# Kernel optimization log

Hardware: AMD Instinct MI355X
Metric: run time of the kernel (lower is better)

The kernel has to match this reference:

```python
import jax, jax.numpy as jnp
import numpy as np

N, D, E = 100000, 128, 800000

def setup_inputs() -> dict:
    key = jax.random.key(0)
    k1, k2, k3, k4 = jax.random.split(key, 4)
    z = jax.random.normal(k1, (N, D), dtype=jnp.float32)
    edge_index = jax.random.randint(k2, (2, E), 0, N, dtype=jnp.int64)
    # PyTorch-style init scale for Linear layers (kaiming-uniform-ish via normal is fine for a numeric reference)
    W1 = jax.random.normal(k3, (2 * D, D), dtype=jnp.float32) * (1.0 / np.sqrt(2 * D))
    b1 = jnp.zeros((D,), dtype=jnp.float32)
    W2 = jax.random.normal(k4, (D, 1), dtype=jnp.float32) * (1.0 / np.sqrt(D))
    b2 = jnp.zeros((1,), dtype=jnp.float32)
    return {"z": z, "edge_index": edge_index, "W1": W1, "b1": b1, "W2": W2, "b2": b2}

def reference(z, edge_index, W1, b1, W2, b2):
    # row/col gather of node embeddings
    row, col = edge_index[0], edge_index[1]
    # cat([z[row], z[col]]) @ W1 == z[row] @ W1[:D] + z[col] @ W1[D:]
    # -> avoids materializing the [E, 2D] concatenated tensor
    d = z.shape[1]
    h = z[row] @ W1[:d] + z[col] @ W1[d:] + b1          # [E, D]
    h = jax.nn.relu(h)                                   # Dropout(0.1) is identity in eval mode
    out = h @ W2 + b2                                    # [E, 1]
    return out.squeeze(-1)                               # [E]
```

## Files before the change

kernel.cpp:

```cpp
#include <hip/hip_runtime.h>

#define DDIM 128

typedef __bf16 bf16x8 __attribute__((ext_vector_type(8)));
typedef float  floatx4 __attribute__((ext_vector_type(4)));

__global__ __launch_bounds__(256, 4) void precompute_uv_mfma_q8(
    const float* __restrict__ z, const float* __restrict__ W1,
    const float* __restrict__ b1,
    unsigned char* __restrict__ U8, unsigned char* __restrict__ V8,
    float* __restrict__ u_scale, float* __restrict__ v_scale,
    int N, int nchunks)
{
    __shared__ unsigned short WsF[32 * 64 * 8];

    const int t    = threadIdx.x;
    const int lane = t & 63;
    const int w    = t >> 6;
    const int half = blockIdx.x;
    unsigned char* __restrict__ dst8 = half ? V8 : U8;
    float*         __restrict__ dscl = half ? v_scale : u_scale;
    const float*   __restrict__ Wh   = W1 + (size_t)half * DDIM * DDIM;

    const int mrow = lane & 15;
    const int quad = lane >> 4;
    const int gy   = gridDim.y;

    float4 rx[8];
    auto issue_loads = [&](int ch) {
        int grow = ch * 64 + w * 16 + mrow;
        if (grow > N - 1) grow = N - 1;
        const float* zrow = z + (size_t)grow * DDIM;
        #pragma unroll
        for (int ks = 0; ks < 4; ++ks) {
            const int k0 = ks * 32 + quad * 8;
            rx[2 * ks]     = *(const float4*)(zrow + k0);
            rx[2 * ks + 1] = *(const float4*)(zrow + k0 + 4);
        }
    };

    if (blockIdx.y < nchunks) issue_loads(blockIdx.y);

    {
        const int nlow = lane & 15;
        const int kq   = (lane >> 4) & 3;
        #pragma unroll
        for (int i = 0; i < 8; ++i) {
            const int ntks = w + i * 4;
            const int nt = ntks >> 2, ks = ntks & 3;
            const int n  = nt * 16 + nlow;
            const int kb = ks * 32 + kq * 8;
            float f[8];
            #pragma unroll
            for (int j = 0; j < 8; ++j)
                f[j] = Wh[(kb + j) * DDIM + n];
            unsigned pk[4];
            #pragma unroll
            for (int j = 0; j < 4; ++j)
                asm("v_cvt_pk_bf16_f32 %0, %1, %2"
                    : "=v"(pk[j]) : "v"(f[2 * j]), "v"(f[2 * j + 1]));
            *(uint4*)&WsF[(ntks * 64 + lane) * 8] = *(const uint4*)pk;
        }
    }

    float bval[8];
    #pragma unroll
    for (int nt = 0; nt < 8; ++nt)
        bval[nt] = (half == 0) ? b1[nt * 16 + mrow] : 0.f;

    __syncthreads();

    for (int chunk = blockIdx.y; chunk < nchunks; chunk += gy) {
        bf16x8 afrag[4];
        #pragma unroll
        for (int ks = 0; ks < 4; ++ks) {
            const float4 x0 = rx[2 * ks];
            const float4 x1 = rx[2 * ks + 1];
            unsigned pk[4];
            asm("v_cvt_pk_bf16_f32 %0, %1, %2" : "=v"(pk[0]) : "v"(x0.x), "v"(x0.y));
            asm("v_cvt_pk_bf16_f32 %0, %1, %2" : "=v"(pk[1]) : "v"(x0.z), "v"(x0.w));
            asm("v_cvt_pk_bf16_f32 %0, %1, %2" : "=v"(pk[2]) : "v"(x1.x), "v"(x1.y));
            asm("v_cvt_pk_bf16_f32 %0, %1, %2" : "=v"(pk[3]) : "v"(x1.z), "v"(x1.w));
            afrag[ks] = __builtin_bit_cast(bf16x8, *(const uint4*)pk);
        }

        const int nxt = chunk + gy;
        if (nxt < nchunks) issue_loads(nxt);

        floatx4 acc[8];
        #pragma unroll
        for (int nt = 0; nt < 8; ++nt)
            acc[nt] = (floatx4){bval[nt], bval[nt], bval[nt], bval[nt]};

        #pragma unroll
        for (int ks = 0; ks < 4; ++ks) {
            #pragma unroll
            for (int nt = 0; nt < 8; ++nt) {
                const bf16x8 b = __builtin_bit_cast(bf16x8,
                    *(const uint4*)&WsF[((nt * 4 + ks) * 64 + lane) * 8]);
                acc[nt] = __builtin_amdgcn_mfma_f32_16x16x32_bf16(afrag[ks], b, acc[nt], 0, 0, 0);
            }
        }

        #pragma unroll
        for (int r = 0; r < 4; ++r) {
            float mx = fmaxf(fmaxf(fabsf(acc[0][r]), fabsf(acc[1][r])),
                             fabsf(acc[2][r]));
            mx = fmaxf(fmaxf(mx, fabsf(acc[3][r])), fabsf(acc[4][r]));
            mx = fmaxf(fmaxf(mx, fabsf(acc[5][r])), fabsf(acc[6][r]));
            mx = fmaxf(mx, fabsf(acc[7][r]));
            #pragma unroll
            for (int m = 1; m < 16; m <<= 1)
                mx = fmaxf(mx, __shfl_xor(mx, m, 16));
            mx = fmaxf(mx, 1e-20f);
            const float inv = 127.f * __builtin_amdgcn_rcpf(mx);

            unsigned char bytes[8];
            #pragma unroll
            for (int nt = 0; nt < 8; ++nt) {
                const float fq = fmaf(acc[nt][r], inv, 12583040.0f);
                bytes[nt] = (unsigned char)(__builtin_bit_cast(unsigned, fq) & 0xffu);
            }
            const int grow = chunk * 64 + w * 16 + quad * 4 + r;
            if (grow < N) {
                *(uint2*)&dst8[(size_t)grow * DDIM + mrow * 8] =
                    *(const uint2*)bytes;
                if (mrow == 0) dscl[grow] = mx * (1.f / 127.f);
            }
        }
    }
}

__global__ __launch_bounds__(256) void edge_kernel_i8(
    const int* __restrict__ ei,
    const unsigned char* __restrict__ U8, const unsigned char* __restrict__ V8,
    const float* __restrict__ u_scale, const float* __restrict__ v_scale,
    const float* __restrict__ W2, const float* __restrict__ b2,
    float* __restrict__ out, int E)
{
    const int t  = threadIdx.x;
    const int q  = t & 7;
    const int g0 = (blockIdx.x * 32 + (t >> 3)) * 4;
    if (g0 >= E) return;

    float ww[16];
    #pragma unroll
    for (int k = 0; k < 16; ++k)
        ww[k] = W2[(k & 7) * 16 + 2 * q + (k >> 3)];

    int rows[4], cols[4];
    if (g0 + 3 < E) {
        const int4 r4 = *(const int4*)(ei + g0);
        const int4 c4 = *(const int4*)(ei + (size_t)E + g0);
        rows[0]=r4.x; rows[1]=r4.y; rows[2]=r4.z; rows[3]=r4.w;
        cols[0]=c4.x; cols[1]=c4.y; cols[2]=c4.z; cols[3]=c4.w;
    } else {
        #pragma unroll
        for (int i = 0; i < 4; ++i) {
            const int gi = (g0 + i < E) ? (g0 + i) : (E - 1);
            rows[i] = ei[gi];
            cols[i] = ei[(size_t)E + gi];
        }
    }

    uint4 uu[4], vv[4];
    #pragma unroll
    for (int i = 0; i < 4; ++i)
        uu[i] = *(const uint4*)(U8 + (size_t)rows[i] * DDIM + q * 16);
    #pragma unroll
    for (int i = 0; i < 4; ++i)
        vv[i] = *(const uint4*)(V8 + (size_t)cols[i] * DDIM + q * 16);

    float su[4], sv[4];
    #pragma unroll
    for (int i = 0; i < 4; ++i) { su[i] = u_scale[rows[i]]; sv[i] = v_scale[cols[i]]; }

    const float bias = b2[0];

    float sres[4];
    #pragma unroll
    for (int i = 0; i < 4; ++i) {
        const unsigned uw0 = uu[i].x, uw1 = uu[i].y, uw2 = uu[i].z, uw3 = uu[i].w;
        const unsigned vw0 = vv[i].x, vw1 = vv[i].y, vw2 = vv[i].z, vw3 = vv[i].w;
        const float c = -128.f * (su[i] + sv[i]);
        float s = 0.f;
        #pragma unroll
        for (int k = 0; k < 16; ++k) {
            const unsigned uwk = (k < 4) ? uw0 : (k < 8) ? uw1 : (k < 12) ? uw2 : uw3;
            const unsigned vwk = (k < 4) ? vw0 : (k < 8) ? vw1 : (k < 12) ? vw2 : vw3;
            const float uf = (float)((uwk >> (8 * (k & 3))) & 0xffu);
            const float vf = (float)((vwk >> (8 * (k & 3))) & 0xffu);
            const float h  = fmaf(su[i], uf, fmaf(sv[i], vf, c));
            s = fmaf(fmaxf(h, 0.f), ww[k], s);
        }
        s += __shfl_down(s, 4, 8);
        s += __shfl_down(s, 2, 8);
        s += __shfl_down(s, 1, 8);
        sres[i] = s + bias;
    }

    if (q == 0) {
        if (g0 + 3 < E) {
            float4 o; o.x = sres[0]; o.y = sres[1]; o.z = sres[2]; o.w = sres[3];
            *(float4*)&out[g0] = o;
        } else {
            #pragma unroll
            for (int i = 0; i < 4; ++i)
                if (g0 + i < E) out[g0 + i] = sres[i];
        }
    }
}

__global__ __launch_bounds__(256) void edge_fused_fallback(
    const float* __restrict__ z, const int* __restrict__ ei,
    const float* __restrict__ W1, const float* __restrict__ b1,
    const float* __restrict__ W2, const float* __restrict__ b2,
    float* __restrict__ out, int N, int E)
{
    const int tid  = blockIdx.x * 256 + threadIdx.x;
    const int e    = tid >> 6;
    const int lane = tid & 63;
    if (e >= E) return;

    const int row = ei[e];
    const int col = ei[(size_t)E + e];
    const float* zr = z + (size_t)row * DDIM;
    const float* zc = z + (size_t)col * DDIM;

    float h0 = b1[lane];
    float h1 = b1[lane + 64];
    for (int k = 0; k < DDIM; ++k) {
        const float a = zr[k];
        const float b = zc[k];
        h0 = fmaf(a, W1[k * DDIM + lane],               h0);
        h0 = fmaf(b, W1[(DDIM + k) * DDIM + lane],      h0);
        h1 = fmaf(a, W1[k * DDIM + lane + 64],          h1);
        h1 = fmaf(b, W1[(DDIM + k) * DDIM + lane + 64], h1);
    }
    float s = fmaxf(h0, 0.f) * W2[lane] + fmaxf(h1, 0.f) * W2[lane + 64];
    #pragma unroll
    for (int off = 32; off > 0; off >>= 1)
        s += __shfl_down(s, off, 64);
    if (lane == 0) out[e] = s + b2[0];
}

extern "C" void kernel_launch(void* const* d_in, const int* in_sizes, int n_in,
                              void* d_out, int out_size, void* d_ws, size_t ws_size,
                              hipStream_t stream)
{
    const float* z  = (const float*)d_in[0];
    const int*   ei = (const int*)d_in[1];
    const float* W1 = (const float*)d_in[2];
    const float* b1 = (const float*)d_in[3];
    const float* W2 = (const float*)d_in[4];
    const float* b2 = (const float*)d_in[5];
    float*       out = (float*)d_out;

    const int N = in_sizes[0] / DDIM;
    const int E = in_sizes[1] / 2;

    const size_t n128 = (size_t)N * DDIM;
    const size_t need = 2 * n128 + 2 * (size_t)N * sizeof(float) + 256;
    if (ws_size >= need) {
        unsigned char* U8 = (unsigned char*)d_ws;
        unsigned char* V8 = U8 + n128;
        float* usc = (float*)(((size_t)(V8 + n128) + 255) & ~(size_t)255);
        float* vsc = usc + N;
        const int nchunks = (N + 63) / 64;
        const int gy = nchunks < 640 ? nchunks : 640;
        hipLaunchKernelGGL(precompute_uv_mfma_q8, dim3(2, gy), dim3(256), 0, stream,
                           z, W1, b1, U8, V8, usc, vsc, N, nchunks);
        hipLaunchKernelGGL(edge_kernel_i8, dim3((E + 127) / 128), dim3(256), 0, stream,
                           ei, U8, V8, usc, vsc, W2, b2, out, E);
    } else {
        hipLaunchKernelGGL(edge_fused_fallback, dim3((E + 3) / 4), dim3(256), 0, stream,
                           z, ei, W1, b1, W2, b2, out, N, E);
    }
}
```

Baseline: 139.7 us.

## Stage z tiles through swizzled LDS for coalesced loads in precompute kernel

```diff
diff --git a/kernel.cpp b/kernel.cpp
--- a/kernel.cpp
+++ b/kernel.cpp
@@ -5,7 +5,7 @@
 typedef __bf16 bf16x8 __attribute__((ext_vector_type(8)));
 typedef float  floatx4 __attribute__((ext_vector_type(4)));
 
-__global__ __launch_bounds__(256, 4) void precompute_uv_mfma_q8(
+__global__ __launch_bounds__(256, 2) void precompute_uv_mfma_q8(
     const float* __restrict__ z, const float* __restrict__ W1,
     const float* __restrict__ b1,
     unsigned char* __restrict__ U8, unsigned char* __restrict__ V8,
@@ -13,6 +13,7 @@
     int N, int nchunks)
 {
     __shared__ unsigned short WsF[32 * 64 * 8];
+    __shared__ float As[4][16][128];
 
     const int t    = threadIdx.x;
     const int lane = t & 63;
@@ -25,17 +26,32 @@
     const int mrow = lane & 15;
     const int quad = lane >> 4;
     const int gy   = gridDim.y;
+    const int rsub = lane >> 3;
+    const int usub = lane & 7;
 
     float4 rx[8];
     auto issue_loads = [&](int ch) {
-        int grow = ch * 64 + w * 16 + mrow;
-        if (grow > N - 1) grow = N - 1;
-        const float* zrow = z + (size_t)grow * DDIM;
-        #pragma unroll
-        for (int ks = 0; ks < 4; ++ks) {
-            const int k0 = ks * 32 + quad * 8;
-            rx[2 * ks]     = *(const float4*)(zrow + k0);
-            rx[2 * ks + 1] = *(const float4*)(zrow + k0 + 4);
+        const int base = ch * 64 + w * 16;
+        #pragma unroll
+        for (int rg = 0; rg < 2; ++rg) {
+            int grow = base + 8 * rg + rsub;
+            if (grow > N - 1) grow = N - 1;
+            const float* zrow = z + (size_t)grow * DDIM;
+            #pragma unroll
+            for (int cq = 0; cq < 4; ++cq)
+                rx[rg * 4 + cq] = *(const float4*)(zrow + cq * 32 + usub * 4);
+        }
+    };
+
+    auto write_tile = [&]() {
+        #pragma unroll
+        for (int rg = 0; rg < 2; ++rg) {
+            const int rl = 8 * rg + rsub;
+            #pragma unroll
+            for (int cq = 0; cq < 4; ++cq) {
+                const int pos = cq * 8 + (usub ^ rsub);
+                *(float4*)&As[w][rl][pos * 4] = rx[rg * 4 + cq];
+            }
         }
     };
 
@@ -71,11 +87,17 @@
     __syncthreads();
 
     for (int chunk = blockIdx.y; chunk < nchunks; chunk += gy) {
+        write_tile();
+        const int nxt = chunk + gy;
+        if (nxt < nchunks) issue_loads(nxt);
+
         bf16x8 afrag[4];
         #pragma unroll
         for (int ks = 0; ks < 4; ++ks) {
-            const float4 x0 = rx[2 * ks];
-            const float4 x1 = rx[2 * ks + 1];
+            const int u0 = ks * 8 + ((quad * 2)     ^ (mrow & 7));
+            const int u1 = ks * 8 + ((quad * 2 + 1) ^ (mrow & 7));
+            const float4 x0 = *(const float4*)&As[w][mrow][u0 * 4];
+            const float4 x1 = *(const float4*)&As[w][mrow][u1 * 4];
             unsigned pk[4];
             asm("v_cvt_pk_bf16_f32 %0, %1, %2" : "=v"(pk[0]) : "v"(x0.x), "v"(x0.y));
             asm("v_cvt_pk_bf16_f32 %0, %1, %2" : "=v"(pk[1]) : "v"(x0.z), "v"(x0.w));
@@ -83,9 +105,6 @@
             asm("v_cvt_pk_bf16_f32 %0, %1, %2" : "=v"(pk[3]) : "v"(x1.z), "v"(x1.w));
             afrag[ks] = __builtin_bit_cast(bf16x8, *(const uint4*)pk);
         }
-
-        const int nxt = chunk + gy;
-        if (nxt < nchunks) issue_loads(nxt);
 
         floatx4 acc[8];
         #pragma unroll
@@ -267,7 +286,7 @@
         float* usc = (float*)(((size_t)(V8 + n128) + 255) & ~(size_t)255);
         float* vsc = usc + N;
         const int nchunks = (N + 63) / 64;
-        const int gy = nchunks < 640 ? nchunks : 640;
+        const int gy = nchunks < 256 ? nchunks : 256;
         hipLaunchKernelGGL(precompute_uv_mfma_q8, dim3(2, gy), dim3(256), 0, stream,
                            z, W1, b1, U8, V8, usc, vsc, N, nchunks);
         hipLaunchKernelGGL(edge_kernel_i8, dim3((E + 127) / 128), dim3(256), 0, stream,
```

Measured after the change: 166.5 us. +19.2%, slower.
